# Performance work log

Measured on AMD Instinct MI355X. Metric: run time of the kernel, lower is better.

Reference implementation:

```python
import jax, jax.numpy as jnp
import numpy as np

H = 16          # num_heads
KVH = 4         # num_kv_heads
HD = 128        # head_dim = dim // num_heads
BASE = 10000.0  # rope_base
EPS = 1.1920928955078125e-07  # torch F.rms_norm default eps = finfo(fp32).eps


def rotate_half(x):
    h = x.shape[-1] // 2
    return jnp.concatenate([-x[..., h:], x[..., :h]], axis=-1)


def rms_norm(x):
    return x * jax.lax.rsqrt(jnp.mean(x * x, axis=-1, keepdims=True) + EPS)


def setup_inputs() -> dict:
    key = jax.random.key(0)
    ks = jax.random.split(key, 5)
    D = H * HD
    KVD = KVH * HD
    s = 0.02
    x = jax.random.normal(ks[0], (4, 2048, D), jnp.float32)
    Wq = jax.random.normal(ks[1], (D, D), jnp.float32) * s
    Wk = jax.random.normal(ks[2], (KVD, D), jnp.float32) * s
    Wv = jax.random.normal(ks[3], (KVD, D), jnp.float32) * s
    Wproj = jax.random.normal(ks[4], (D, D), jnp.float32) * s
    q_gain = jnp.full((H,), 1.0, jnp.float32)
    return {"x": x, "Wq": Wq, "Wk": Wk, "Wv": Wv, "Wproj": Wproj, "q_gain": q_gain}


def reference(x, Wq, Wk, Wv, Wproj, q_gain):
    B, T, D = x.shape
    # QKV projections (bias-free), reshape to [B, heads, T, head_dim]
    q = (x @ Wq.T).reshape(B, T, H, HD).transpose(0, 2, 1, 3)
    k = (x @ Wk.T).reshape(B, T, KVH, HD).transpose(0, 2, 1, 3)
    v = (x @ Wv.T).reshape(B, T, KVH, HD).transpose(0, 2, 1, 3)
    # QK RMSNorm (no learned weight)
    q = rms_norm(q)
    k = rms_norm(k)
    # Rotary embedding tables [T, HD]
    t = jnp.arange(T, dtype=jnp.float32)
    inv_freq = 1.0 / (BASE ** (jnp.arange(0, HD, 2, dtype=jnp.float32) / HD))
    freqs = jnp.outer(t, inv_freq)
    emb = jnp.concatenate([freqs, freqs], axis=-1)
    cos, sin = jnp.cos(emb), jnp.sin(emb)
    # RoPE + per-head gain on q
    q = (q * cos + rotate_half(q) * sin) * q_gain[None, :, None, None]
    k = k * cos + rotate_half(k) * sin
    # GQA: repeat_interleave kv heads to match q heads
    groups = H // KVH
    k = jnp.repeat(k, groups, axis=1)
    v = jnp.repeat(v, groups, axis=1)
    # Causal scaled dot-product attention
    scores = jnp.einsum('bhqd,bhkd->bhqk', q, k) / np.float32(np.sqrt(HD))
    mask = jnp.tril(jnp.ones((T, T), dtype=bool))
    scores = jnp.where(mask, scores, -jnp.inf)
    attn = jax.nn.softmax(scores, axis=-1)
    y = jnp.einsum('bhqk,bhkd->bhqd', attn, v)
    y = y.transpose(0, 2, 1, 3).reshape(B, T, D)
    return y @ Wproj.T
```

## Files before the change

kernel.cpp:

```cpp
#include <hip/hip_runtime.h>
#include <math.h>


typedef float f32x4 __attribute__((ext_vector_type(4)));
typedef __bf16 bf16x8 __attribute__((ext_vector_type(8)));
typedef __bf16 bf16x4 __attribute__((ext_vector_type(4)));
typedef __bf16 bf16x2 __attribute__((ext_vector_type(2)));

__device__ __forceinline__ void load_lds16(const __bf16* g, __bf16* l) {
    __builtin_amdgcn_global_load_lds(
        (const __attribute__((address_space(1))) void*)g,
        (__attribute__((address_space(3))) void*)l, 16, 0, 0);
}

__device__ __forceinline__ unsigned pack_bf16(float lo, float hi) {
    union { bf16x2 v; unsigned u; } c;
    c.v = bf16x2{(__bf16)lo, (__bf16)hi};
    return c.u;
}

__global__ __launch_bounds__(256) void cvt_all(
    const float* __restrict__ x,  const float* __restrict__ Wq,
    const float* __restrict__ Wk, const float* __restrict__ Wv,
    const float* __restrict__ Wp, __bf16* __restrict__ dst)
{
    long long i = ((long long)blockIdx.x * 256 + threadIdx.x) * 4;
    if (i >= 27262976LL) return;
    const float* src;
    long long off;
    if (i < 16777216LL)      { src = x;  off = i; }
    else if (i < 20971520LL) { src = Wq; off = i - 16777216LL; }
    else if (i < 22020096LL) { src = Wk; off = i - 20971520LL; }
    else if (i < 23068672LL) { src = Wv; off = i - 22020096LL; }
    else                     { src = Wp; off = i - 23068672LL; }
    float4 v = *(const float4*)(src + off);
    bf16x4 o = {(__bf16)v.x, (__bf16)v.y, (__bf16)v.z, (__bf16)v.w};
    *(bf16x4*)(dst + i) = o;
}

template <int NI, typename OutT>
__global__ __launch_bounds__(512, 2) void gemm4buf(
    const __bf16* __restrict__ A, const __bf16* __restrict__ W,
    OutT* __restrict__ C, int M, int N, int K)
{
    constexpr int BN = 64 * NI;
    constexpr int WN = 16 * NI;
    const int bm = blockIdx.x, bn = blockIdx.y;
    const int tid = threadIdx.x;
    const int lane = tid & 63;
    const int wave = tid >> 6;
    const int quad = lane >> 4, l16 = lane & 15;
    const int wm2 = wave >> 2;
    const int wn4 = wave & 3;

    __shared__ __bf16 As[4][256 * 32];
    __shared__ __bf16 Bs[4][BN * 32];

    f32x4 acc[8][NI] = {};

    const int sr = tid >> 2;
    const int sc = tid & 3;
    const int scs = sc ^ (sr & 3) ^ ((sr >> 2) & 3);
    const int swzq = quad ^ (l16 & 3) ^ ((l16 >> 2) & 3);

    const __bf16* Ag = A + (size_t)(bm * 256 + sr) * K + scs * 8;
    const __bf16* Wg = W + (size_t)(bn * BN + sr) * K + scs * 8;
    const int dA = sr * 32 + sc * 8;

    auto stageB = [&](int t) {
        const int k0 = t * 32, buf = t & 3;
        load_lds16(Wg + k0, &Bs[buf][dA]);
        if constexpr (NI == 4)
            load_lds16(Wg + (size_t)128 * K + k0, &Bs[buf][128 * 32 + dA]);
    };
    auto stageA = [&](int t) {
        const int k0 = t * 32, buf = t & 3;
        load_lds16(Ag + k0, &As[buf][dA]);
        load_lds16(Ag + (size_t)128 * K + k0, &As[buf][128 * 32 + dA]);
    };
    auto waitAhead = [&](int ahead) {
        if constexpr (NI == 4) {
            if (ahead >= 2)      asm volatile("s_waitcnt vmcnt(8)" ::: "memory");
            else if (ahead == 1) asm volatile("s_waitcnt vmcnt(4)" ::: "memory");
            else                 asm volatile("s_waitcnt vmcnt(0)" ::: "memory");
        } else {
            if (ahead >= 2)      asm volatile("s_waitcnt vmcnt(6)" ::: "memory");
            else if (ahead == 1) asm volatile("s_waitcnt vmcnt(3)" ::: "memory");
            else                 asm volatile("s_waitcnt vmcnt(0)" ::: "memory");
        }
    };

    const int NT = K / 32;

    stageB(0); stageA(0);
    stageB(1); stageA(1);
    stageB(2); stageA(2);
    waitAhead(2);
    asm volatile("" ::: "memory");
    __builtin_amdgcn_s_barrier();
    asm volatile("" ::: "memory");

    for (int t = 0; t < NT; ++t) {
        const __bf16* Ab = &As[t & 3][0];
        const __bf16* Bb = &Bs[t & 3][0];
        const bool pf = (t + 3 < NT);

        bf16x8 bfr[NI];
#pragma unroll
        for (int ni = 0; ni < NI; ++ni)
            bfr[ni] = *(const bf16x8*)(
                Bb + (wn4 * WN + ni * 16 + l16) * 32 + swzq * 8);
        if (pf) stageB(t + 3);

        bf16x8 af[8];
#pragma unroll
        for (int mi = 0; mi < 8; ++mi)
            af[mi] = *(const bf16x8*)(
                Ab + (wm2 * 128 + mi * 16 + l16) * 32 + swzq * 8);
        if (pf) stageA(t + 3);

        __builtin_amdgcn_s_setprio(1);
#pragma unroll
        for (int mi = 0; mi < 8; ++mi)
#pragma unroll
            for (int ni = 0; ni < NI; ++ni)
                acc[mi][ni] = __builtin_amdgcn_mfma_f32_16x16x32_bf16(
                    af[mi], bfr[ni], acc[mi][ni], 0, 0, 0);
        __builtin_amdgcn_s_setprio(0);

        if (t + 1 < NT) {
            const int hi = (t + 3 < NT - 1) ? (t + 3) : (NT - 1);
            waitAhead(hi - (t + 1));
            asm volatile("" ::: "memory");
            __builtin_amdgcn_s_barrier();
            asm volatile("" ::: "memory");
        }
    }

#pragma unroll
    for (int mi = 0; mi < 8; ++mi) {
#pragma unroll
        for (int r = 0; r < 4; ++r) {
            int row = bm * 256 + wm2 * 128 + mi * 16 + quad * 4 + r;
            OutT* Cp = C + (size_t)row * N + bn * BN + wn4 * WN + l16;
#pragma unroll
            for (int ni = 0; ni < NI; ++ni)
                Cp[ni * 16] = (OutT)acc[mi][ni][r];
        }
    }
}

__global__ __launch_bounds__(256) void k_norm_rope(__bf16* __restrict__ kv)
{
    const int row = blockIdx.x * 4 + (threadIdx.x >> 6);
    const int lane = threadIdx.x & 63;
    const int bt = row >> 2, kvh = row & 3;
    __bf16* base = kv + (size_t)bt * 1024 + kvh * 128;
    const int t = bt & 2047;

    float x0 = (float)base[lane];
    float x1 = (float)base[lane + 64];

    float ss = x0 * x0 + x1 * x1;
#pragma unroll
    for (int off = 32; off; off >>= 1) ss += __shfl_xor(ss, off);
    float inv = rsqrtf(ss * (1.0f / 128.0f) + 1.1920928955078125e-07f);
    x0 *= inv; x1 *= inv;

    float freq = exp2f(-(float)lane * 0.20762050593046013f);
    float s, c;
    __sincosf((float)t * freq, &s, &c);
    base[lane]      = (__bf16)(x0 * c - x1 * s);
    base[lane + 64] = (__bf16)(x1 * c + x0 * s);
}

__global__ __launch_bounds__(256) void transpose_v(
    const __bf16* __restrict__ kv, __bf16* __restrict__ vtout)
{
    __shared__ __bf16 tile[64][65];
    const int b = blockIdx.z;
    const int t0 = blockIdx.x * 64, c0 = blockIdx.y * 64;
    const __bf16* vb = kv + (size_t)b * 2048 * 1024 + 512;
    __bf16* vtb = vtout + (size_t)b * 512 * 2048;
    const int j = threadIdx.x & 63;
    const int r0 = threadIdx.x >> 6;
#pragma unroll
    for (int i = 0; i < 16; ++i) {
        int r = r0 + i * 4;
        tile[r][j] = vb[(size_t)(t0 + r) * 1024 + c0 + j];
    }
    __syncthreads();
#pragma unroll
    for (int i = 0; i < 16; ++i) {
        int r = r0 + i * 4;
        vtb[(size_t)(c0 + r) * 2048 + t0 + j] = tile[j][r];
    }
}

__global__ __launch_bounds__(256, 2) void attn(
    const __bf16* __restrict__ q, const __bf16* __restrict__ kv,
    const __bf16* __restrict__ vt, __bf16* __restrict__ y,
    const float* __restrict__ q_gain)
{
    const int qt = 15 - blockIdx.y;
    const int bx = blockIdx.x;
    const int g = bx & 15, j = bx >> 4;
    const int b = g >> 2, kvh = g & 3, h = kvh * 4 + j;
    const int tid = threadIdx.x;
    const int wave = tid >> 6, lane = tid & 63;
    const int quad = lane >> 4, l16 = lane & 15;

    __shared__ __bf16 Ks[2][64 * 128];
    __shared__ __bf16 Vts[2][128 * 64];
    __shared__ unsigned Ppk[2][4][16 * 32];

    const int qt0 = qt * 128;
    const int wq = wave * 16;
    const float gain = q_gain[h];

    bf16x8 qraw[2][4];
#pragma unroll
    for (int p = 0; p < 2; ++p) {
        const size_t qrow =
            ((size_t)b * 2048 + qt0 + p * 64 + wq + l16) * 2048 + h * 128;
#pragma unroll
        for (int t = 0; t < 4; ++t)
            qraw[p][t] = *(const bf16x8*)(q + qrow + t * 32 + quad * 8);
    }

    const size_t kbase = (size_t)b * 2048 * 1024 + kvh * 128;
    const size_t vtbase = (size_t)(b * 4 + kvh) * 128 * 2048;
    const int rowK = lane >> 4, pcK = lane & 15;
    const int rowV = lane >> 3, pcV = lane & 7;
    const int nj = 2 * qt + 2;

    {
#pragma unroll
        for (int r = 0; r < 4; ++r) {
            int rrK = (r * 4 + wave) * 4 + rowK;
            int cK = pcK ^ (rrK & 15);
            load_lds16(kv + kbase + (size_t)rrK * 1024 + cK * 8,
                       &Ks[0][(r * 4 + wave) * 512]);
            int rrV = (r * 4 + wave) * 8 + rowV;
            int cV = pcV ^ (rrV & 7);
            load_lds16(vt + vtbase + (size_t)rrV * 2048 + cV * 8,
                       &Vts[0][(r * 4 + wave) * 512]);
        }
    }

    bf16x8 qf[2][4];
#pragma unroll
    for (int p = 0; p < 2; ++p) {
        float xv[4][8];
        float ss = 0.f;
#pragma unroll
        for (int t = 0; t < 4; ++t)
#pragma unroll
            for (int jj = 0; jj < 8; ++jj) {
                float f = (float)qraw[p][t][jj];
                xv[t][jj] = f; ss += f * f;
            }
        ss += __shfl_xor(ss, 16);
        ss += __shfl_xor(ss, 32);
        const float sc = rsqrtf(ss * (1.0f / 128.0f) +
                                1.1920928955078125e-07f) * gain;
        const float trow = (float)(qt0 + p * 64 + wq + l16);
#pragma unroll
        for (int t = 0; t < 2; ++t)
#pragma unroll
            for (int jj = 0; jj < 8; ++jj) {
                const float fr =
                    exp2f(-(float)(t * 32 + quad * 8 + jj) * 0.20762050593046013f);
                float s, c;
                __sincosf(trow * fr, &s, &c);
                const float x0 = xv[t][jj], x1 = xv[t + 2][jj];
                qf[p][t][jj]     = (__bf16)((x0 * c - x1 * s) * sc);
                qf[p][t + 2][jj] = (__bf16)((x1 * c + x0 * s) * sc);
            }
    }

    f32x4 oacc[2][8] = {};
    float lsum[2] = {0.f, 0.f};
    const float sm_scale = 0.12754635f;
    const float mfix = 11.5f * fabsf(gain);

    for (int jt = 0; jt < nj; ++jt) {
        const int cur = jt & 1;

        asm volatile("" ::: "memory");
        __builtin_amdgcn_s_barrier();
        asm volatile("" ::: "memory");

        if (jt + 1 < nj) {
            const int j0n = (jt + 1) * 64;
#pragma unroll
            for (int r = 0; r < 4; ++r) {
                int rrK = (r * 4 + wave) * 4 + rowK;
                int cK = pcK ^ (rrK & 15);
                load_lds16(kv + kbase + (size_t)(j0n + rrK) * 1024 + cK * 8,
                           &Ks[cur ^ 1][(r * 4 + wave) * 512]);
                int rrV = (r * 4 + wave) * 8 + rowV;
                int cV = pcV ^ (rrV & 7);
                load_lds16(vt + vtbase + (size_t)rrV * 2048 + j0n + cV * 8,
                           &Vts[cur ^ 1][(r * 4 + wave) * 512]);
            }
            asm volatile("s_waitcnt vmcnt(8)" ::: "memory");
        } else {
            asm volatile("s_waitcnt vmcnt(0)" ::: "memory");
        }

        asm volatile("" ::: "memory");
        __builtin_amdgcn_s_barrier();
        asm volatile("" ::: "memory");

        const __bf16* Kc = Ks[cur];
        const __bf16* Vc = Vts[cur];

        f32x4 sacc[2][4] = {};
        __builtin_amdgcn_s_setprio(1);
#pragma unroll
        for (int nt = 0; nt < 4; ++nt)
#pragma unroll
            for (int t = 0; t < 4; ++t) {
                bf16x8 kf = *(const bf16x8*)(
                    Kc + (nt * 16 + l16) * 128 + ((t * 4 + quad) ^ l16) * 8);
                sacc[0][nt] = __builtin_amdgcn_mfma_f32_16x16x32_bf16(
                    kf, qf[0][t], sacc[0][nt], 0, 0, 0);
                sacc[1][nt] = __builtin_amdgcn_mfma_f32_16x16x32_bf16(
                    kf, qf[1][t], sacc[1][nt], 0, 0, 0);
            }
        __builtin_amdgcn_s_setprio(0);

        if (jt >= 2 * qt) {
            const int dj = jt - 2 * qt;
#pragma unroll
            for (int p = 0; p < 2; ++p) {
                const int rel = (p - dj) * 64 + wq + l16;
#pragma unroll
                for (int nt = 0; nt < 4; ++nt) {
                    const int kvb = nt * 16 + quad * 4;
#pragma unroll
                    for (int r = 0; r < 4; ++r)
                        if (kvb + r > rel) sacc[p][nt][r] = -3.0e38f;
                }
            }
        }

#pragma unroll
        for (int p = 0; p < 2; ++p) {
            unsigned* Pw = &Ppk[p][wave][0];
            const int wb = l16 * 32 + (quad & 1) * 2;
            float ls = 0.f;
#pragma unroll
            for (int nt = 0; nt < 4; ++nt) {
                float e0 = exp2f((sacc[p][nt][0] - mfix) * sm_scale);
                float e1 = exp2f((sacc[p][nt][1] - mfix) * sm_scale);
                float e2 = exp2f((sacc[p][nt][2] - mfix) * sm_scale);
                float e3 = exp2f((sacc[p][nt][3] - mfix) * sm_scale);
                ls += (e0 + e1) + (e2 + e3);
                uint2 u;
                u.x = pack_bf16(e0, e1);
                u.y = pack_bf16(e2, e3);
                *(uint2*)(Pw + wb + (((nt * 2 + (quad >> 1)) ^ (l16 & 7)) << 2)) = u;
            }
            lsum[p] += ls;
        }

        __builtin_amdgcn_s_setprio(1);
#pragma unroll
        for (int kt = 0; kt < 2; ++kt) {
            const int pcc = (kt * 4 + quad) ^ (l16 & 7);
            union { uint4 u; bf16x8 v; } c0, c1;
            c0.u = *(const uint4*)(&Ppk[0][wave][0] + l16 * 32 + (pcc << 2));
            c1.u = *(const uint4*)(&Ppk[1][wave][0] + l16 * 32 + (pcc << 2));
#pragma unroll
            for (int vn = 0; vn < 8; ++vn) {
                bf16x8 vf = *(const bf16x8*)(
                    Vc + (vn * 16 + l16) * 64 + pcc * 8);
                oacc[0][vn] = __builtin_amdgcn_mfma_f32_16x16x32_bf16(
                    vf, c0.v, oacc[0][vn], 0, 0, 0);
                oacc[1][vn] = __builtin_amdgcn_mfma_f32_16x16x32_bf16(
                    vf, c1.v, oacc[1][vn], 0, 0, 0);
            }
        }
        __builtin_amdgcn_s_setprio(0);
    }

#pragma unroll
    for (int p = 0; p < 2; ++p) {
        lsum[p] += __shfl_xor(lsum[p], 16);
        lsum[p] += __shfl_xor(lsum[p], 32);
        const float inv = 1.0f / lsum[p];
        const size_t ybase =
            ((size_t)b * 2048 + qt0 + p * 64 + wq + l16) * 2048 +
            h * 128 + quad * 4;
#pragma unroll
        for (int vn = 0; vn < 8; ++vn) {
            bf16x4 o = {(__bf16)(oacc[p][vn][0] * inv),
                        (__bf16)(oacc[p][vn][1] * inv),
                        (__bf16)(oacc[p][vn][2] * inv),
                        (__bf16)(oacc[p][vn][3] * inv)};
            *(bf16x4*)(y + ybase + vn * 16) = o;
        }
    }
}

extern "C" void kernel_launch(void* const* d_in, const int* in_sizes, int n_in,
                              void* d_out, int out_size, void* d_ws, size_t ws_size,
                              hipStream_t stream) {
    const float* x     = (const float*)d_in[0];
    const float* Wq    = (const float*)d_in[1];
    const float* Wk    = (const float*)d_in[2];
    const float* Wv    = (const float*)d_in[3];
    const float* Wproj = (const float*)d_in[4];
    const float* qgain = (const float*)d_in[5];
    float* outp = (float*)d_out;

    __bf16* xb  = (__bf16*)d_ws;
    __bf16* Wqb = xb  + 16777216;
    __bf16* Wkb = Wqb + 4194304;
    __bf16* Wvb = Wkb + 1048576;
    __bf16* Wpb = Wvb + 1048576;
    __bf16* q   = Wpb + 4194304;
    __bf16* kvb = q   + 16777216;
    __bf16* vt  = kvb + 8388608;
    __bf16* y   = q;

    dim3 blk(256);
    cvt_all<<<dim3(27262976 / 1024), blk, 0, stream>>>(x, Wq, Wk, Wv, Wproj, xb);

    gemm4buf<4, __bf16><<<dim3(32, 8), dim3(512), 0, stream>>>(xb, Wqb, q, 8192, 2048, 2048);
    gemm4buf<2, __bf16><<<dim3(32, 8), dim3(512), 0, stream>>>(xb, Wkb, kvb, 8192, 1024, 2048);
    k_norm_rope<<<dim3((4 * 2048 * 4) / 4), blk, 0, stream>>>(kvb);
    transpose_v<<<dim3(32, 8, 4), blk, 0, stream>>>(kvb, vt);
    attn<<<dim3(64, 16), blk, 0, stream>>>(q, kvb, vt, y, qgain);
    gemm4buf<4, float><<<dim3(32, 8), dim3(512), 0, stream>>>(y, Wpb, outp, 8192, 2048, 2048);
}
```

Measured before the change: 454.5 us.

## Add 8-phase double-buffered GEMM with interleaved loads for Q and output projections

Adds a new 256x256-tile GEMM kernel with K-step 64, two LDS buffers and an 8-phase schedule. Each phase issues a slice of the next tiles' global-to-LDS loads, then runs an MFMA batch under raised wave priority between barriers. It replaces the 4-buffer GEMM for the Q projection and the output projection. The goal is better overlap of memory traffic with MFMA work and fewer LDS stalls. The cost is many more barriers per K-tile and tight vmcnt accounting that must stay correct.

Measured after the change: 451.9 us (median of 2 runs). About the same (-0.6%).

```diff
diff --git a/kernel.cpp b/kernel.cpp
--- a/kernel.cpp
+++ b/kernel.cpp
@@ -36,6 +36,124 @@
     float4 v = *(const float4*)(src + off);
     bf16x4 o = {(__bf16)v.x, (__bf16)v.y, (__bf16)v.z, (__bf16)v.w};
     *(bf16x4*)(dst + i) = o;
+}
+
+template <typename OutT>
+__global__ __launch_bounds__(512, 2) void gemm8ph(
+    const __bf16* __restrict__ A, const __bf16* __restrict__ W,
+    OutT* __restrict__ C, int M, int N, int K)
+{
+    const int bm = blockIdx.x, bn = blockIdx.y;
+    const int tid = threadIdx.x;
+    const int lane = tid & 63, wave = tid >> 6;
+    const int quad = lane >> 4, l16 = lane & 15;
+    const int wm2 = wave >> 2;
+    const int wn4 = wave & 3;
+
+    __shared__ __bf16 As[2][256 * 64];
+    __shared__ __bf16 Bs[2][256 * 64];
+
+    f32x4 acc[8][4] = {};
+
+    const int sr = tid >> 3;
+    const int sc = tid & 7;
+    const int scs = sc ^ (((sr >> 2) & 1) << 1);
+    const __bf16* Ag = A + (size_t)(bm * 256 + sr) * K + scs * 8;
+    const __bf16* Wg = W + (size_t)(bn * 256 + sr) * K + scs * 8;
+    const int dst = sr * 64 + sc * 8;
+
+    auto stA = [&](int t, int r) {
+        load_lds16(Ag + (size_t)(r * 64) * K + t * 64,
+                   &As[t & 1][r * 4096 + dst]);
+    };
+    auto stB = [&](int t, int r) {
+        load_lds16(Wg + (size_t)(r * 64) * K + t * 64,
+                   &Bs[t & 1][r * 4096 + dst]);
+    };
+
+    const int NT = K / 64;
+    const int swzr = ((l16 >> 2) & 1) << 1;
+
+#pragma unroll
+    for (int r = 0; r < 4; ++r) { stA(0, r); stB(0, r); }
+#pragma unroll
+    for (int r = 0; r < 4; ++r) { stA(1, r); stB(1, r); }
+    asm volatile("s_waitcnt vmcnt(8)" ::: "memory");
+    __builtin_amdgcn_s_barrier();
+
+    bf16x8 bfr[4][2];
+
+    for (int i = 0; i < NT / 2; ++i) {
+        const int t0 = 2 * i;
+#pragma unroll
+        for (int tt = 0; tt < 2; ++tt) {
+            const __bf16* Ab = &As[tt][0];
+            const __bf16* Bb = &Bs[tt][0];
+#pragma unroll
+            for (int qq = 0; qq < 4; ++qq) {
+                bf16x8 af[2][2];
+#pragma unroll
+                for (int j = 0; j < 2; ++j)
+#pragma unroll
+                    for (int ks = 0; ks < 2; ++ks)
+                        af[j][ks] = *(const bf16x8*)(
+                            Ab + (wm2 * 128 + (qq * 2 + j) * 16 + l16) * 64 +
+                            ((ks * 4 + quad) ^ swzr) * 8);
+                if (qq == 0) {
+#pragma unroll
+                    for (int ni = 0; ni < 4; ++ni)
+#pragma unroll
+                        for (int ks = 0; ks < 2; ++ks)
+                            bfr[ni][ks] = *(const bf16x8*)(
+                                Bb + (wn4 * 64 + ni * 16 + l16) * 64 +
+                                ((ks * 4 + quad) ^ swzr) * 8);
+                }
+
+                const int p = tt * 4 + qq;
+                switch (p) {
+                    case 0: if (i > 0) { stA(t0 + 1, 1); stA(t0 + 1, 3); } break;
+                    case 1: if (t0 + 2 < NT) { stB(t0 + 2, 0); stB(t0 + 2, 1); } break;
+                    case 2: if (t0 + 2 < NT) { stA(t0 + 2, 0); stA(t0 + 2, 2); } break;
+                    case 3: if (t0 + 2 < NT) { stB(t0 + 2, 2); stB(t0 + 2, 3); } break;
+                    case 4: if (t0 + 2 < NT) { stA(t0 + 2, 1); stA(t0 + 2, 3); } break;
+                    case 5: if (t0 + 3 < NT) { stB(t0 + 3, 0); stB(t0 + 3, 1); } break;
+                    case 6: if (t0 + 3 < NT) { stA(t0 + 3, 0); stA(t0 + 3, 2); } break;
+                    case 7: if (t0 + 3 < NT) { stB(t0 + 3, 2); stB(t0 + 3, 3); } break;
+                }
+                if (qq == 3)
+                    asm volatile("s_waitcnt vmcnt(6)" ::: "memory");
+
+                __builtin_amdgcn_s_barrier();
+                asm volatile("s_waitcnt lgkmcnt(0)" ::: "memory");
+                __builtin_amdgcn_sched_barrier(0);
+                __builtin_amdgcn_s_setprio(1);
+#pragma unroll
+                for (int j = 0; j < 2; ++j)
+#pragma unroll
+                    for (int ni = 0; ni < 4; ++ni)
+#pragma unroll
+                        for (int ks = 0; ks < 2; ++ks)
+                            acc[qq * 2 + j][ni] =
+                                __builtin_amdgcn_mfma_f32_16x16x32_bf16(
+                                    af[j][ks], bfr[ni][ks],
+                                    acc[qq * 2 + j][ni], 0, 0, 0);
+                __builtin_amdgcn_s_setprio(0);
+                __builtin_amdgcn_s_barrier();
+            }
+        }
+    }
+
+#pragma unroll
+    for (int mi = 0; mi < 8; ++mi) {
+#pragma unroll
+        for (int r = 0; r < 4; ++r) {
+            int row = bm * 256 + wm2 * 128 + mi * 16 + quad * 4 + r;
+            OutT* Cp = C + (size_t)row * N + bn * 256 + wn4 * 64 + l16;
+#pragma unroll
+            for (int ni = 0; ni < 4; ++ni)
+                Cp[ni * 16] = (OutT)acc[mi][ni][r];
+        }
+    }
 }
 
 template <int NI, typename OutT>
@@ -429,10 +547,10 @@
     dim3 blk(256);
     cvt_all<<<dim3(27262976 / 1024), blk, 0, stream>>>(x, Wq, Wk, Wv, Wproj, xb);
 
-    gemm4buf<4, __bf16><<<dim3(32, 8), dim3(512), 0, stream>>>(xb, Wqb, q, 8192, 2048, 2048);
+    gemm8ph<__bf16><<<dim3(32, 8), dim3(512), 0, stream>>>(xb, Wqb, q, 8192, 2048, 2048);
     gemm4buf<2, __bf16><<<dim3(32, 8), dim3(512), 0, stream>>>(xb, Wkb, kvb, 8192, 1024, 2048);
     k_norm_rope<<<dim3((4 * 2048 * 4) / 4), blk, 0, stream>>>(kvb);
     transpose_v<<<dim3(32, 8, 4), blk, 0, stream>>>(kvb, vt);
     attn<<<dim3(64, 16), blk, 0, stream>>>(q, kvb, vt, y, qgain);
-    gemm4buf<4, float><<<dim3(32, 8), dim3(512), 0, stream>>>(y, Wpb, outp, 8192, 2048, 2048);
-}
+    gemm8ph<float><<<dim3(32, 8), dim3(512), 0, stream>>>(y, Wpb, outp, 8192, 2048, 2048);
+}
```
